# Optimization experiments

Hardware: AMD Instinct MI355X
Metric: run time of the kernel (lower is better)

## Reference

```python
import jax, jax.numpy as jnp
import numpy as np

N_NODES = 10000
N_EDGES = 640000
N_GRAPHS = 100
D_FEAT = 128
D_HID = 512


def setup_inputs() -> dict:
    key = jax.random.key(0)
    ks = jax.random.split(key, 6)
    nodes = jax.random.normal(ks[0], (N_NODES, D_FEAT), jnp.float32)
    edges = jax.random.uniform(ks[1], (N_EDGES, 1), jnp.float32)  # per-edge regularization weight
    senders = jax.random.randint(ks[2], (N_EDGES,), 0, N_NODES, jnp.int32)
    receivers = jax.random.randint(ks[3], (N_EDGES,), 0, N_NODES, jnp.int32)
    n_node = jnp.full((N_GRAPHS,), N_NODES // N_GRAPHS, jnp.int32)
    n_edge = jnp.full((N_GRAPHS,), N_EDGES // N_GRAPHS, jnp.int32)
    W1 = jax.random.normal(ks[4], (D_FEAT, D_HID), jnp.float32) / np.float32(np.sqrt(D_FEAT))
    b1 = jnp.zeros((D_HID,), jnp.float32)
    W2 = jax.random.normal(ks[5], (D_HID, D_FEAT), jnp.float32) / np.float32(np.sqrt(D_HID))
    b2 = jnp.zeros((D_FEAT,), jnp.float32)
    return dict(nodes=nodes, edges=edges, senders=senders, receivers=receivers,
                n_node=n_node, n_edge=n_edge, W1=W1, b1=b1, W2=W2, b2=b2)


def reference(nodes, edges, senders, receivers, n_node, n_edge, W1, b1, W2, b2):
    G = n_node.shape[0]
    E = edges.shape[0]
    # graph id for each edge (EdgesToGlobalsAggregator segment ids)
    edge_gid = jnp.repeat(jnp.arange(G, dtype=jnp.int32), n_edge, total_repeat_length=E)
    w = edges[:, 0]  # [E] edge weights
    # example_weights = unsorted_segment_sum of edge features per graph
    example_weights = jax.ops.segment_sum(w, edge_gid, num_segments=G)  # [G]
    # GraphIndependent node model: MLP applied per node
    h = jax.nn.relu(nodes @ W1 + b1) @ W2 + b2  # [N, D]
    # EdgeRelationNetwork edge block: gather sender/receiver features, weighted L2 distance
    src = jnp.take(h, senders, axis=0)     # [E, D]
    dst = jnp.take(h, receivers, axis=0)   # [E, D]
    edge_out = w * jnp.sum(jnp.square(src - dst), axis=-1)  # [E]
    # aggregate edges -> globals (unsorted_segment_sum)
    globals_agg = jax.ops.segment_sum(edge_out, edge_gid, num_segments=G)  # [G]
    # graph loss: mean(divide_no_nan(globals, example_weights))
    graph_loss = jnp.mean(jnp.where(example_weights != 0.0,
                                    globals_agg / jnp.where(example_weights != 0.0, example_weights, 1.0),
                                    0.0))
    # NodeGraphModel output: node features at last node of each graph
    node_ids = jnp.cumsum(n_node) - 1  # [G]
    node_out = jnp.take(h, node_ids, axis=0)  # [G, D]
    return node_out, graph_loss
```

## Files before the change

kernel.cpp:

```cpp
#include <hip/hip_runtime.h>

#define D_F 128
#define D_H 512
#define SHS 520

typedef short v8s __attribute__((ext_vector_type(8)));
typedef float v4f __attribute__((ext_vector_type(4)));
typedef _Float16 v2h __attribute__((ext_vector_type(2)));

__device__ inline unsigned short f2bf(float f) {
    unsigned u = __float_as_uint(f);
    unsigned r = (u + 0x7fffu + ((u >> 16) & 1u)) >> 16;
    return (unsigned short)r;
}
__device__ inline v2h bch(unsigned x) { return __builtin_bit_cast(v2h, x); }

__global__ __launch_bounds__(256) void prep_kernel(
    const float* __restrict__ W1, const float* __restrict__ W2,
    const int* __restrict__ n_node, const int* __restrict__ n_edge,
    unsigned short* __restrict__ W1T, unsigned short* __restrict__ W2T,
    int* __restrict__ ec, int* __restrict__ nid,
    float* __restrict__ ew, float* __restrict__ ga, int G, int E)
{
    if (blockIdx.x == 0) {
        __shared__ int sne[512];
        __shared__ int snn[512];
        const int t = threadIdx.x;
        for (int g = t; g < G; g += 256) { sne[g] = n_edge[g]; snn[g] = n_node[g]; }
        __syncthreads();
        for (int g = t; g < G; g += 256) {
            int se = 0, sn = 0;
            for (int k = 0; k < g; ++k)  se += sne[k];
            for (int k = 0; k <= g; ++k) sn += snn[k];
            ec[g]  = se;
            nid[g] = sn - 1;
            ew[g] = 0.f;
            ga[g] = 0.f;
            if (g == G - 1) {
                int tot = se + sne[g];
                ec[G] = tot > E ? tot : E;
            }
        }
    }
    int i = blockIdx.x * 256 + threadIdx.x;
    if (i < D_F * D_H) {
        int n = i >> 7, k = i & (D_F - 1);
        W1T[i] = f2bf(W1[k * D_H + n]);
        int n2 = i >> 9, k2 = i & (D_H - 1);
        W2T[i] = f2bf(W2[k2 * D_F + n2]);
    }
}

__global__ __launch_bounds__(512) void mlp_mfma_kernel(
    const float* __restrict__ nodes,
    const unsigned short* __restrict__ W1T, const float* __restrict__ b1,
    const unsigned short* __restrict__ W2T, const float* __restrict__ b2,
    _Float16* __restrict__ hh, int N)
{
    __shared__ unsigned short sH[32 * SHS];

    const int t    = threadIdx.x;
    const int wave = t >> 6;
    const int lane = t & 63;
    const int li   = lane & 15;
    const int quad = lane >> 4;
    const int row0 = blockIdx.x * 32;

    v8s a1[2][4];
    #pragma unroll
    for (int rg = 0; rg < 2; ++rg) {
        int r = min(row0 + rg * 16 + li, N - 1);
        const float* xp = nodes + (size_t)r * D_F + quad * 8;
        #pragma unroll
        for (int ks = 0; ks < 4; ++ks) {
            float4 f0 = *(const float4*)(xp + ks * 32);
            float4 f1 = *(const float4*)(xp + ks * 32 + 4);
            v8s v;
            v[0] = (short)f2bf(f0.x); v[1] = (short)f2bf(f0.y);
            v[2] = (short)f2bf(f0.z); v[3] = (short)f2bf(f0.w);
            v[4] = (short)f2bf(f1.x); v[5] = (short)f2bf(f1.y);
            v[6] = (short)f2bf(f1.z); v[7] = (short)f2bf(f1.w);
            a1[rg][ks] = v;
        }
    }

    #pragma unroll 2
    for (int jj = 0; jj < 4; ++jj) {
        const int n0 = (wave * 4 + jj) * 16;
        const unsigned short* wp = W1T + (size_t)(n0 + li) * D_F + quad * 8;
        v4f acc0 = {0.f, 0.f, 0.f, 0.f};
        v4f acc1 = {0.f, 0.f, 0.f, 0.f};
        #pragma unroll
        for (int ks = 0; ks < 4; ++ks) {
            v8s b = *(const v8s*)(wp + ks * 32);
            acc0 = __builtin_amdgcn_mfma_f32_16x16x32_bf16(a1[0][ks], b, acc0, 0, 0, 0);
            acc1 = __builtin_amdgcn_mfma_f32_16x16x32_bf16(a1[1][ks], b, acc1, 0, 0, 0);
        }
        float bias = b1[n0 + li];
        #pragma unroll
        for (int r = 0; r < 4; ++r) {
            int m = quad * 4 + r;
            sH[m * SHS + n0 + li]        = f2bf(fmaxf(acc0[r] + bias, 0.f));
            sH[(16 + m) * SHS + n0 + li] = f2bf(fmaxf(acc1[r] + bias, 0.f));
        }
    }
    __syncthreads();

    {
        const int n0 = wave * 16;
        const unsigned short* wp = W2T + (size_t)(n0 + li) * D_H + quad * 8;
        v4f acc0 = {0.f, 0.f, 0.f, 0.f};
        v4f acc1 = {0.f, 0.f, 0.f, 0.f};
        #pragma unroll
        for (int kc = 0; kc < 4; ++kc) {
            v8s bb[4], aH0[4], aH1[4];
            #pragma unroll
            for (int u = 0; u < 4; ++u) {
                int ks = kc * 4 + u;
                bb[u]  = *(const v8s*)(wp + ks * 32);
                aH0[u] = *(const v8s*)(sH + li * SHS + ks * 32 + quad * 8);
                aH1[u] = *(const v8s*)(sH + (16 + li) * SHS + ks * 32 + quad * 8);
            }
            #pragma unroll
            for (int u = 0; u < 4; ++u) {
                acc0 = __builtin_amdgcn_mfma_f32_16x16x32_bf16(aH0[u], bb[u], acc0, 0, 0, 0);
                acc1 = __builtin_amdgcn_mfma_f32_16x16x32_bf16(aH1[u], bb[u], acc1, 0, 0, 0);
            }
        }
        float bias = b2[n0 + li];
        #pragma unroll
        for (int r = 0; r < 4; ++r) {
            int g0 = row0 + quad * 4 + r;
            if (g0 < N) hh[(size_t)g0 * D_F + n0 + li] = (_Float16)(acc0[r] + bias);
            int g1 = row0 + 16 + quad * 4 + r;
            if (g1 < N) hh[(size_t)g1 * D_F + n0 + li] = (_Float16)(acc1[r] + bias);
        }
    }
}

__global__ __launch_bounds__(512) void edge_kernel(
    const _Float16* __restrict__ hh, const float* __restrict__ wedge,
    const int* __restrict__ senders, const int* __restrict__ receivers,
    const int* __restrict__ ec,
    float* __restrict__ ew, float* __restrict__ ga,
    int E, int G)
{
    __shared__ int   sec[513];
    __shared__ float sga[512];
    __shared__ float sew[512];
    const int t = threadIdx.x;
    for (int i = t; i <= G; i += 512) sec[i] = ec[i];
    for (int i = t; i < G;  i += 512) { sga[i] = 0.f; sew[i] = 0.f; }
    __syncthreads();

    const unsigned* __restrict__ h32 = (const unsigned*)hh;
    const uint4*    __restrict__ h16 = (const uint4*)hh;
    const int lane = t & 63;
    const int tb   = (blockIdx.x * 8 + (t >> 6)) << 6;

    if (tb < E) {
        const int tbu = __builtin_amdgcn_readfirstlane(tb);
        const int nt  = min(64, E - tbu);

        int gid;
        { int lo = 0, hi = G - 1;
          while (lo < hi) { int m = (lo + hi + 1) >> 1; if (sec[m] <= tbu) lo = m; else hi = m - 1; }
          gid = lo; }

        const int*   __restrict__ sp = senders   + tbu;
        const int*   __restrict__ rp = receivers + tbu;
        const float* __restrict__ wp = wedge     + tbu;

        if (nt == 64 && tbu + 64 <= sec[gid + 1]) {
            const bool q0 = (lane & 16) != 0;
            const bool q1 = (lane & 32) != 0;
            const int  c  = lane & 15;
            float accE = 0.f, accW = 0.f;
            #pragma unroll 1
            for (int i = 0; i < 64; i += 32) {
                uint4 a[8], b[8];
                #pragma unroll
                for (int u = 0; u < 8; ++u) {
                    int e = i + u * 4;
                    int s0 = sp[e], s1 = sp[e + 1], s2 = sp[e + 2], s3 = sp[e + 3];
                    int r0 = rp[e], r1 = rp[e + 1], r2 = rp[e + 2], r3 = rp[e + 3];
                    int sA = q0 ? s1 : s0;
                    int sB = q0 ? s3 : s2;
                    int s  = q1 ? sB : sA;
                    int rA = q0 ? r1 : r0;
                    int rB = q0 ? r3 : r2;
                    int r  = q1 ? rB : rA;
                    a[u] = h16[(unsigned)((s << 4) | c)];
                    b[u] = h16[(unsigned)((r << 4) | c)];
                }
                #pragma unroll
                for (int u = 0; u < 8; ++u) {
                    int e = i + u * 4;
                    float w0 = wp[e], w1 = wp[e + 1], w2 = wp[e + 2], w3 = wp[e + 3];
                    float wA = q0 ? w1 : w0;
                    float wB = q0 ? w3 : w2;
                    float w  = q1 ? wB : wA;
                    v2h d0 = bch(a[u].x) - bch(b[u].x);
                    v2h d1 = bch(a[u].y) - bch(b[u].y);
                    v2h d2 = bch(a[u].z) - bch(b[u].z);
                    v2h d3 = bch(a[u].w) - bch(b[u].w);
                    float tt = __builtin_amdgcn_fdot2(d0, d0, 0.f, false);
                    tt = __builtin_amdgcn_fdot2(d1, d1, tt, false);
                    tt = __builtin_amdgcn_fdot2(d2, d2, tt, false);
                    tt = __builtin_amdgcn_fdot2(d3, d3, tt, false);
                    accE = fmaf(w, tt, accE);
                    accW += w;
                }
            }
            float rE = accE, rW = accW;
            #pragma unroll
            for (int m = 32; m > 0; m >>= 1) {
                rE += __shfl_xor(rE, m);
                rW += __shfl_xor(rW, m);
            }
            if (lane == 0) {
                atomicAdd(&sga[gid], rE);
                atomicAdd(&sew[gid], rW * 0.0625f);
            }
        } else {
            float accE = 0.f, accW = 0.f;
            for (int i = 0; i < nt; ++i) {
                int e = tbu + i;
                while (e >= sec[gid + 1]) {
                    float rE = accE;
                    #pragma unroll
                    for (int m = 32; m > 0; m >>= 1) rE += __shfl_xor(rE, m);
                    if (lane == 0 && (rE != 0.f || accW != 0.f)) {
                        atomicAdd(&sga[gid], rE);
                        atomicAdd(&sew[gid], accW);
                    }
                    accE = 0.f; accW = 0.f;
                    ++gid;
                }
                int   s = sp[i];
                int   r = rp[i];
                float w = wp[i];
                unsigned a = h32[(unsigned)((s << 6) | lane)];
                unsigned b = h32[(unsigned)((r << 6) | lane)];
                v2h d = bch(a) - bch(b);
                float tt = __builtin_amdgcn_fdot2(d, d, 0.f, false);
                accE = fmaf(w, tt, accE);
                accW += w;
            }
            float rE = accE;
            #pragma unroll
            for (int m = 32; m > 0; m >>= 1) rE += __shfl_xor(rE, m);
            if (lane == 0 && (rE != 0.f || accW != 0.f)) {
                atomicAdd(&sga[gid], rE);
                atomicAdd(&sew[gid], accW);
            }
        }
    }

    __syncthreads();
    for (int g = t; g < G; g += 512) {
        float vg = sga[g], vw = sew[g];
        if (vg != 0.f || vw != 0.f) {
            atomicAdd(&ga[g], vg);
            atomicAdd(&ew[g], vw);
        }
    }
}

__global__ __launch_bounds__(128) void finalize_kernel(
    const _Float16* __restrict__ hh, const int* __restrict__ nid,
    const float* __restrict__ ew, const float* __restrict__ ga,
    float* __restrict__ out, int G)
{
    const int g = blockIdx.x;
    const int t = threadIdx.x;
    if (g < G) {
        int src = nid[g];
        out[(size_t)g * D_F + t] = (float)hh[(size_t)src * D_F + t];
    } else {
        float p = 0.f;
        for (int i = t; i < G; i += 128) {
            float w = ew[i];
            p += (w != 0.f) ? ga[i] / w : 0.f;
        }
        #pragma unroll
        for (int m = 32; m > 0; m >>= 1) p += __shfl_xor(p, m);
        __shared__ float sp[2];
        if ((t & 63) == 0) sp[t >> 6] = p;
        __syncthreads();
        if (t == 0) out[(size_t)G * D_F] = (sp[0] + sp[1]) / (float)G;
    }
}

extern "C" void kernel_launch(void* const* d_in, const int* in_sizes, int n_in,
                              void* d_out, int out_size, void* d_ws, size_t ws_size,
                              hipStream_t stream) {
    const float* nodes     = (const float*)d_in[0];
    const float* edges     = (const float*)d_in[1];
    const int*   senders   = (const int*)d_in[2];
    const int*   receivers = (const int*)d_in[3];
    const int*   n_node    = (const int*)d_in[4];
    const int*   n_edge    = (const int*)d_in[5];
    const float* W1        = (const float*)d_in[6];
    const float* b1        = (const float*)d_in[7];
    const float* W2        = (const float*)d_in[8];
    const float* b2        = (const float*)d_in[9];

    const int N = in_sizes[0] / D_F;
    const int E = in_sizes[1];
    const int G = in_sizes[4];

    float* out = (float*)d_out;

    _Float16*       hh  = (_Float16*)d_ws;
    unsigned short* W1T = (unsigned short*)(hh + (size_t)N * D_F);
    unsigned short* W2T = W1T + (size_t)D_F * D_H;
    int*            ec  = (int*)(W2T + (size_t)D_F * D_H);
    int*            nid = ec + (G + 1);
    float*          ew  = (float*)(nid + G);
    float*          ga  = ew + G;

    prep_kernel<<<(D_F * D_H + 255) / 256, 256, 0, stream>>>(
        W1, W2, n_node, n_edge, W1T, W2T, ec, nid, ew, ga, G, E);

    const int nblk = (N + 31) / 32;
    mlp_mfma_kernel<<<nblk, 512, 0, stream>>>(nodes, W1T, b1, W2T, b2, hh, N);

    const int ntiles = (E + 63) / 64;
    const int nblkE  = (ntiles + 7) / 8;
    edge_kernel<<<nblkE, 512, 0, stream>>>(hh, edges, senders, receivers, ec,
                                           ew, ga, E, G);

    finalize_kernel<<<G + 1, 128, 0, stream>>>(hh, nid, ew, ga, out, G);
}
```

Baseline: 128.6 us.

## Fuse MLP, edge and finalize kernels into one persistent kernel with grid barrier

Replaces the separate MLP, edge-loss and finalize launches with a single persistent kernel of fixed grid size. Blocks loop over the MLP tiles, meet at an atomic-counter grid barrier, then loop over the edge tiles. The last block to finish runs the finalize step. This removes two kernel launches and their gaps. The cost is a software grid barrier that relies on all blocks being co-resident, and less parallelism in the MLP phase. The second GEMM inner loop is also re-chunked from 4 to 2 loads per stage.

```diff
diff --git a/kernel.cpp b/kernel.cpp
--- a/kernel.cpp
+++ b/kernel.cpp
@@ -3,6 +3,7 @@
 #define D_F 128
 #define D_H 512
 #define SHS 520
+#define NGRID 512
 
 typedef short v8s __attribute__((ext_vector_type(8)));
 typedef float v4f __attribute__((ext_vector_type(4)));
@@ -20,12 +21,14 @@
     const int* __restrict__ n_node, const int* __restrict__ n_edge,
     unsigned short* __restrict__ W1T, unsigned short* __restrict__ W2T,
     int* __restrict__ ec, int* __restrict__ nid,
-    float* __restrict__ ew, float* __restrict__ ga, int G, int E)
+    float* __restrict__ ew, float* __restrict__ ga,
+    int* __restrict__ bar, int G, int E)
 {
     if (blockIdx.x == 0) {
         __shared__ int sne[512];
         __shared__ int snn[512];
         const int t = threadIdx.x;
+        if (t < 2) bar[t] = 0;
         for (int g = t; g < G; g += 256) { sne[g] = n_edge[g]; snn[g] = n_node[g]; }
         __syncthreads();
         for (int g = t; g < G; g += 256) {
@@ -51,115 +54,124 @@
     }
 }
 
-__global__ __launch_bounds__(512) void mlp_mfma_kernel(
+__global__ __launch_bounds__(512, 4) void mega_kernel(
     const float* __restrict__ nodes,
     const unsigned short* __restrict__ W1T, const float* __restrict__ b1,
     const unsigned short* __restrict__ W2T, const float* __restrict__ b2,
-    _Float16* __restrict__ hh, int N)
+    _Float16* __restrict__ hh,
+    const float* __restrict__ wedge,
+    const int* __restrict__ senders, const int* __restrict__ receivers,
+    const int* __restrict__ ec, const int* __restrict__ nid,
+    float* __restrict__ ew, float* __restrict__ ga,
+    int* __restrict__ bar, float* __restrict__ out,
+    int N, int E, int G, int nblk, int ntiles)
 {
-    __shared__ unsigned short sH[32 * SHS];
+    __shared__ __align__(16) char smem[32 * SHS * 2];
+    unsigned short* sH = (unsigned short*)smem;
 
     const int t    = threadIdx.x;
     const int wave = t >> 6;
     const int lane = t & 63;
     const int li   = lane & 15;
     const int quad = lane >> 4;
-    const int row0 = blockIdx.x * 32;
-
-    v8s a1[2][4];
-    #pragma unroll
-    for (int rg = 0; rg < 2; ++rg) {
-        int r = min(row0 + rg * 16 + li, N - 1);
-        const float* xp = nodes + (size_t)r * D_F + quad * 8;
+
+    for (int tile = blockIdx.x; tile < nblk; tile += NGRID) {
+        const int row0 = tile * 32;
+
+        v8s a1[2][4];
         #pragma unroll
-        for (int ks = 0; ks < 4; ++ks) {
-            float4 f0 = *(const float4*)(xp + ks * 32);
-            float4 f1 = *(const float4*)(xp + ks * 32 + 4);
-            v8s v;
-            v[0] = (short)f2bf(f0.x); v[1] = (short)f2bf(f0.y);
-            v[2] = (short)f2bf(f0.z); v[3] = (short)f2bf(f0.w);
-            v[4] = (short)f2bf(f1.x); v[5] = (short)f2bf(f1.y);
-            v[6] = (short)f2bf(f1.z); v[7] = (short)f2bf(f1.w);
-            a1[rg][ks] = v;
-        }
-    }
-
-    #pragma unroll 2
-    for (int jj = 0; jj < 4; ++jj) {
-        const int n0 = (wave * 4 + jj) * 16;
-        const unsigned short* wp = W1T + (size_t)(n0 + li) * D_F + quad * 8;
-        v4f acc0 = {0.f, 0.f, 0.f, 0.f};
-        v4f acc1 = {0.f, 0.f, 0.f, 0.f};
-        #pragma unroll
-        for (int ks = 0; ks < 4; ++ks) {
-            v8s b = *(const v8s*)(wp + ks * 32);
-            acc0 = __builtin_amdgcn_mfma_f32_16x16x32_bf16(a1[0][ks], b, acc0, 0, 0, 0);
-            acc1 = __builtin_amdgcn_mfma_f32_16x16x32_bf16(a1[1][ks], b, acc1, 0, 0, 0);
-        }
-        float bias = b1[n0 + li];
-        #pragma unroll
-        for (int r = 0; r < 4; ++r) {
-            int m = quad * 4 + r;
-            sH[m * SHS + n0 + li]        = f2bf(fmaxf(acc0[r] + bias, 0.f));
-            sH[(16 + m) * SHS + n0 + li] = f2bf(fmaxf(acc1[r] + bias, 0.f));
-        }
-    }
-    __syncthreads();
-
-    {
-        const int n0 = wave * 16;
-        const unsigned short* wp = W2T + (size_t)(n0 + li) * D_H + quad * 8;
-        v4f acc0 = {0.f, 0.f, 0.f, 0.f};
-        v4f acc1 = {0.f, 0.f, 0.f, 0.f};
-        #pragma unroll
-        for (int kc = 0; kc < 4; ++kc) {
-            v8s bb[4], aH0[4], aH1[4];
-            #pragma unroll
-            for (int u = 0; u < 4; ++u) {
-                int ks = kc * 4 + u;
-                bb[u]  = *(const v8s*)(wp + ks * 32);
-                aH0[u] = *(const v8s*)(sH + li * SHS + ks * 32 + quad * 8);
-                aH1[u] = *(const v8s*)(sH + (16 + li) * SHS + ks * 32 + quad * 8);
-            }
-            #pragma unroll
-            for (int u = 0; u < 4; ++u) {
-                acc0 = __builtin_amdgcn_mfma_f32_16x16x32_bf16(aH0[u], bb[u], acc0, 0, 0, 0);
-                acc1 = __builtin_amdgcn_mfma_f32_16x16x32_bf16(aH1[u], bb[u], acc1, 0, 0, 0);
-            }
-        }
-        float bias = b2[n0 + li];
-        #pragma unroll
-        for (int r = 0; r < 4; ++r) {
-            int g0 = row0 + quad * 4 + r;
-            if (g0 < N) hh[(size_t)g0 * D_F + n0 + li] = (_Float16)(acc0[r] + bias);
-            int g1 = row0 + 16 + quad * 4 + r;
-            if (g1 < N) hh[(size_t)g1 * D_F + n0 + li] = (_Float16)(acc1[r] + bias);
-        }
-    }
-}
-
-__global__ __launch_bounds__(512) void edge_kernel(
-    const _Float16* __restrict__ hh, const float* __restrict__ wedge,
-    const int* __restrict__ senders, const int* __restrict__ receivers,
-    const int* __restrict__ ec,
-    float* __restrict__ ew, float* __restrict__ ga,
-    int E, int G)
-{
-    __shared__ int   sec[513];
-    __shared__ float sga[512];
-    __shared__ float sew[512];
-    const int t = threadIdx.x;
+        for (int rg = 0; rg < 2; ++rg) {
+            int r = min(row0 + rg * 16 + li, N - 1);
+            const float* xp = nodes + (size_t)r * D_F + quad * 8;
+            #pragma unroll
+            for (int ks = 0; ks < 4; ++ks) {
+                float4 f0 = *(const float4*)(xp + ks * 32);
+                float4 f1 = *(const float4*)(xp + ks * 32 + 4);
+                v8s v;
+                v[0] = (short)f2bf(f0.x); v[1] = (short)f2bf(f0.y);
+                v[2] = (short)f2bf(f0.z); v[3] = (short)f2bf(f0.w);
+                v[4] = (short)f2bf(f1.x); v[5] = (short)f2bf(f1.y);
+                v[6] = (short)f2bf(f1.z); v[7] = (short)f2bf(f1.w);
+                a1[rg][ks] = v;
+            }
+        }
+
+        #pragma unroll 2
+        for (int jj = 0; jj < 4; ++jj) {
+            const int n0 = (wave * 4 + jj) * 16;
+            const unsigned short* wp = W1T + (size_t)(n0 + li) * D_F + quad * 8;
+            v4f acc0 = {0.f, 0.f, 0.f, 0.f};
+            v4f acc1 = {0.f, 0.f, 0.f, 0.f};
+            #pragma unroll
+            for (int ks = 0; ks < 4; ++ks) {
+                v8s b = *(const v8s*)(wp + ks * 32);
+                acc0 = __builtin_amdgcn_mfma_f32_16x16x32_bf16(a1[0][ks], b, acc0, 0, 0, 0);
+                acc1 = __builtin_amdgcn_mfma_f32_16x16x32_bf16(a1[1][ks], b, acc1, 0, 0, 0);
+            }
+            float bias = b1[n0 + li];
+            #pragma unroll
+            for (int r = 0; r < 4; ++r) {
+                int m = quad * 4 + r;
+                sH[m * SHS + n0 + li]        = f2bf(fmaxf(acc0[r] + bias, 0.f));
+                sH[(16 + m) * SHS + n0 + li] = f2bf(fmaxf(acc1[r] + bias, 0.f));
+            }
+        }
+        __syncthreads();
+
+        {
+            const int n0 = wave * 16;
+            const unsigned short* wp = W2T + (size_t)(n0 + li) * D_H + quad * 8;
+            v4f acc0 = {0.f, 0.f, 0.f, 0.f};
+            v4f acc1 = {0.f, 0.f, 0.f, 0.f};
+            #pragma unroll
+            for (int kc = 0; kc < 8; ++kc) {
+                v8s bb[2], aH0[2], aH1[2];
+                #pragma unroll
+                for (int u = 0; u < 2; ++u) {
+                    int ks = kc * 2 + u;
+                    bb[u]  = *(const v8s*)(wp + ks * 32);
+                    aH0[u] = *(const v8s*)(sH + li * SHS + ks * 32 + quad * 8);
+                    aH1[u] = *(const v8s*)(sH + (16 + li) * SHS + ks * 32 + quad * 8);
+                }
+                #pragma unroll
+                for (int u = 0; u < 2; ++u) {
+                    acc0 = __builtin_amdgcn_mfma_f32_16x16x32_bf16(aH0[u], bb[u], acc0, 0, 0, 0);
+                    acc1 = __builtin_amdgcn_mfma_f32_16x16x32_bf16(aH1[u], bb[u], acc1, 0, 0, 0);
+                }
+            }
+            float bias = b2[n0 + li];
+            #pragma unroll
+            for (int r = 0; r < 4; ++r) {
+                int g0 = row0 + quad * 4 + r;
+                if (g0 < N) hh[(size_t)g0 * D_F + n0 + li] = (_Float16)(acc0[r] + bias);
+                int g1 = row0 + 16 + quad * 4 + r;
+                if (g1 < N) hh[(size_t)g1 * D_F + n0 + li] = (_Float16)(acc1[r] + bias);
+            }
+        }
+        __syncthreads();
+    }
+
+    __threadfence();
+    __syncthreads();
+    if (t == 0) {
+        atomicAdd(&bar[0], 1);
+        while (atomicAdd(&bar[0], 0) < (int)gridDim.x) __builtin_amdgcn_s_sleep(2);
+    }
+    __syncthreads();
+    __threadfence();
+
+    int*   sec = (int*)smem;
+    float* sga = (float*)(smem + 2112);
+    float* sew = sga + 512;
     for (int i = t; i <= G; i += 512) sec[i] = ec[i];
     for (int i = t; i < G;  i += 512) { sga[i] = 0.f; sew[i] = 0.f; }
     __syncthreads();
 
     const unsigned* __restrict__ h32 = (const unsigned*)hh;
     const uint4*    __restrict__ h16 = (const uint4*)hh;
-    const int lane = t & 63;
-    const int tb   = (blockIdx.x * 8 + (t >> 6)) << 6;
-
-    if (tb < E) {
-        const int tbu = __builtin_amdgcn_readfirstlane(tb);
+
+    for (int tile = blockIdx.x * 8 + wave; tile < ntiles; tile += NGRID * 8) {
+        const int tbu = __builtin_amdgcn_readfirstlane(tile << 6);
         const int nt  = min(64, E - tbu);
 
         int gid;
@@ -265,30 +277,35 @@
             atomicAdd(&ew[g], vw);
         }
     }
-}
-
-__global__ __launch_bounds__(128) void finalize_kernel(
-    const _Float16* __restrict__ hh, const int* __restrict__ nid,
-    const float* __restrict__ ew, const float* __restrict__ ga,
-    float* __restrict__ out, int G)
-{
-    const int g = blockIdx.x;
-    const int t = threadIdx.x;
-    if (g < G) {
-        int src = nid[g];
-        out[(size_t)g * D_F + t] = (float)hh[(size_t)src * D_F + t];
-    } else {
+
+    __threadfence();
+    __syncthreads();
+    if (t == 0) {
+        int old = atomicAdd(&bar[1], 1);
+        sec[0] = (old == (int)gridDim.x - 1) ? 1 : 0;
+    }
+    __syncthreads();
+    if (sec[0]) {
+        for (int i = t; i < G * D_F; i += 512) {
+            int g = i >> 7, c = i & (D_F - 1);
+            out[i] = (float)hh[(size_t)nid[g] * D_F + c];
+        }
         float p = 0.f;
-        for (int i = t; i < G; i += 128) {
-            float w = ew[i];
-            p += (w != 0.f) ? ga[i] / w : 0.f;
+        for (int g = t; g < G; g += 512) {
+            float w = atomicAdd(&ew[g], 0.f);
+            float v = atomicAdd(&ga[g], 0.f);
+            p += (w != 0.f) ? v / w : 0.f;
         }
         #pragma unroll
         for (int m = 32; m > 0; m >>= 1) p += __shfl_xor(p, m);
-        __shared__ float sp[2];
-        if ((t & 63) == 0) sp[t >> 6] = p;
+        if (lane == 0) sga[wave] = p;
         __syncthreads();
-        if (t == 0) out[(size_t)G * D_F] = (sp[0] + sp[1]) / (float)G;
+        if (t == 0) {
+            float s = 0.f;
+            #pragma unroll
+            for (int w = 0; w < 8; ++w) s += sga[w];
+            out[(size_t)G * D_F] = s / (float)G;
+        }
     }
 }
 
@@ -319,17 +336,15 @@
     int*            nid = ec + (G + 1);
     float*          ew  = (float*)(nid + G);
     float*          ga  = ew + G;
+    int*            bar = (int*)(ga + G);
 
     prep_kernel<<<(D_F * D_H + 255) / 256, 256, 0, stream>>>(
-        W1, W2, n_node, n_edge, W1T, W2T, ec, nid, ew, ga, G, E);
-
-    const int nblk = (N + 31) / 32;
-    mlp_mfma_kernel<<<nblk, 512, 0, stream>>>(nodes, W1T, b1, W2T, b2, hh, N);
-
+        W1, W2, n_node, n_edge, W1T, W2T, ec, nid, ew, ga, bar, G, E);
+
+    const int nblk   = (N + 31) / 32;
     const int ntiles = (E + 63) / 64;
-    const int nblkE  = (ntiles + 7) / 8;
-    edge_kernel<<<nblkE, 512, 0, stream>>>(hh, edges, senders, receivers, ec,
-                                           ew, ga, E, G);
-
-    finalize_kernel<<<G + 1, 128, 0, stream>>>(hh, nid, ew, ga, out, G);
+
+    mega_kernel<<<NGRID, 512, 0, stream>>>(
+        nodes, W1T, b1, W2T, b2, hh, edges, senders, receivers,
+        ec, nid, ew, ga, bar, out, N, E, G, nblk, ntiles);
 }
```

Result: slower. 376.0 us (+192.4%).
